# Performance work log

Measured on AMD Instinct MI355X. Metric: run time of the kernel, lower is better.

Reference implementation:

```python
import jax, jax.numpy as jnp
import numpy as np

EPS = 1e-8
MASK_MIN = 0.0


def setup_inputs() -> dict:
    key = jax.random.key(0)
    k1, k2, k3, k4 = jax.random.split(key, 4)
    B, H, CELLS, W = 8, 8, 8192, 256
    memory = jax.random.normal(k1, (B, CELLS, W), dtype=jnp.float32)
    keys = jax.random.normal(k2, (B, H, W), dtype=jnp.float32)
    betas = jax.random.uniform(k3, (B, H), dtype=jnp.float32)
    mask = jax.random.uniform(k4, (B, H, W), dtype=jnp.float32)
    return {"memory": memory, "keys": keys, "betas": betas, "mask": mask}


def reference(memory, keys, betas, mask):
    # memory: [B, C, W]; keys: [B, H, W]; betas: [B, H]; mask: [B, H, W]
    mask = mask * (1.0 - MASK_MIN) + MASK_MIN
    m2 = mask * mask                                   # [B, H, W]
    keys_m = keys * mask                               # masked keys
    # (memory*mask) . (keys*mask) summed over W == memory . (keys*mask^2)
    dots = jnp.einsum('bcw,bhw->bhc', memory, keys * m2)        # [B, H, C]
    keys_norm = jnp.linalg.norm(keys_m, axis=-1)                # [B, H]
    mem_norm = jnp.sqrt(jnp.einsum('bcw,bhw->bhc', memory * memory, m2))  # [B, H, C]
    norm = keys_norm[..., None] * mem_norm                      # [B, H, C]
    scores = dots / (norm + EPS) * betas[..., None]
    return jax.nn.softmax(scores, axis=-1)                      # [B, H, C]
```

## Files before the change

kernel.cpp:

```cpp
#include <hip/hip_runtime.h>
#include <cstdint>
#include <cmath>

#define EPS_F 1e-8f

constexpr int B = 8, H = 8, CELLS = 8192, W = 256;
constexpr int W4 = 64;
constexpr int TC = 32;
constexpr int NBLK = CELLS / TC;

template <int CTRL>
__device__ __forceinline__ float ror_add(float v) {
    int x = __builtin_amdgcn_update_dpp(0, __builtin_bit_cast(int, v),
                                        CTRL, 0xf, 0xf, false);
    return v + __builtin_bit_cast(float, x);
}
__device__ __forceinline__ float row_sum16(float v) {
    v = ror_add<0x121>(v);
    v = ror_add<0x122>(v);
    v = ror_add<0x124>(v);
    v = ror_add<0x128>(v);
    return v;
}

#define GLOAD_LDS16(g, l)                                                    \
    __builtin_amdgcn_global_load_lds(                                        \
        (__attribute__((address_space(1))) void*)(void*)(g),                 \
        (__attribute__((address_space(3))) void*)(l), 16, 0, 0)

__global__ __launch_bounds__(256, 3) void ca_scores(
    const float4* __restrict__ mem4,
    const float4* __restrict__ keys4,
    const float4* __restrict__ mask4,
    const float* __restrict__ betas,
    float* __restrict__ out,
    float2* __restrict__ part)
{
    __shared__ float4 s_tile[TC * W4];
    __shared__ float  s_sc[H][TC + 1];
    __shared__ float  s_fin[H], s_sum2[H];

    const int b = blockIdx.y, blk = blockIdx.x, t = threadIdx.x;
    const int c0 = blk * TC;
    const int lane = t & 63, wv = t >> 6;
    const int hp  = (lane >> 4) & 3;
    const int wsl = lane & 15;

    const float4* __restrict__ kA = keys4 + ((size_t)(b * 8 + hp)) * W4;
    const float4* __restrict__ mA = mask4 + ((size_t)(b * 8 + hp)) * W4;
    const float4* __restrict__ kB = keys4 + ((size_t)(b * 8 + hp + 4)) * W4;
    const float4* __restrict__ mB = mask4 + ((size_t)(b * 8 + hp + 4)) * W4;
    float4 ka[4], ma[4], kb[4], mb[4];
#pragma unroll
    for (int j = 0; j < 4; ++j) {
        ka[j] = kA[j * 16 + wsl];  ma[j] = mA[j * 16 + wsl];
        kb[j] = kB[j * 16 + wsl];  mb[j] = mB[j * 16 + wsl];
    }
    const float beA = betas[b * 8 + hp];
    const float beB = betas[b * 8 + hp + 4];

    const float4* __restrict__ gbase = mem4 + ((size_t)b * CELLS + c0) * W4;
#pragma unroll
    for (int i = 0; i < 8; ++i)
        GLOAD_LDS16(gbase + t + i * 256, &s_tile[t + i * 256]);

    float4 tb[16];
    float pA = 0.f, pB = 0.f;
#pragma unroll
    for (int j = 0; j < 4; ++j) {
        float4 m = ma[j];
        float4 q = make_float4(m.x * m.x, m.y * m.y, m.z * m.z, m.w * m.w);
        float4 k = ka[j];
        tb[j * 4 + 0] = make_float4(k.x * q.x, k.y * q.y, k.z * q.z, k.w * q.w);
        tb[j * 4 + 1] = q;
        float km;
        km = k.x * m.x; pA = fmaf(km, km, pA);
        km = k.y * m.y; pA = fmaf(km, km, pA);
        km = k.z * m.z; pA = fmaf(km, km, pA);
        km = k.w * m.w; pA = fmaf(km, km, pA);
        m = mb[j];
        q = make_float4(m.x * m.x, m.y * m.y, m.z * m.z, m.w * m.w);
        k = kb[j];
        tb[j * 4 + 2] = make_float4(k.x * q.x, k.y * q.y, k.z * q.z, k.w * q.w);
        tb[j * 4 + 3] = q;
        km = k.x * m.x; pB = fmaf(km, km, pB);
        km = k.y * m.y; pB = fmaf(km, km, pB);
        km = k.z * m.z; pB = fmaf(km, km, pB);
        km = k.w * m.w; pB = fmaf(km, km, pB);
    }
    const float knA = sqrtf(row_sum16(pA));
    const float knB = sqrtf(row_sum16(pB));

    __syncthreads();

#pragma unroll
    for (int c = 0; c < 8; ++c) {
        const int cell = wv * 8 + c;
        const float4* __restrict__ pr = s_tile + cell * W4 + wsl;
        float4 a0 = pr[0], a1 = pr[16], a2 = pr[32], a3 = pr[48];

        float4 dA = make_float4(0.f, 0.f, 0.f, 0.f);
        float4 nA = make_float4(0.f, 0.f, 0.f, 0.f);
        float4 dB = make_float4(0.f, 0.f, 0.f, 0.f);
        float4 nB = make_float4(0.f, 0.f, 0.f, 0.f);

#define ACC(a, j)                                                           \
        {                                                                   \
            float4 sq = make_float4(a.x * a.x, a.y * a.y, a.z * a.z, a.w * a.w); \
            float4 kqA = tb[(j) * 4 + 0], qA = tb[(j) * 4 + 1];             \
            float4 kqB = tb[(j) * 4 + 2], qB = tb[(j) * 4 + 3];             \
            dA.x = fmaf(a.x, kqA.x, dA.x); dA.y = fmaf(a.y, kqA.y, dA.y);   \
            dA.z = fmaf(a.z, kqA.z, dA.z); dA.w = fmaf(a.w, kqA.w, dA.w);   \
            nA.x = fmaf(sq.x, qA.x, nA.x); nA.y = fmaf(sq.y, qA.y, nA.y);   \
            nA.z = fmaf(sq.z, qA.z, nA.z); nA.w = fmaf(sq.w, qA.w, nA.w);   \
            dB.x = fmaf(a.x, kqB.x, dB.x); dB.y = fmaf(a.y, kqB.y, dB.y);   \
            dB.z = fmaf(a.z, kqB.z, dB.z); dB.w = fmaf(a.w, kqB.w, dB.w);   \
            nB.x = fmaf(sq.x, qB.x, nB.x); nB.y = fmaf(sq.y, qB.y, nB.y);   \
            nB.z = fmaf(sq.z, qB.z, nB.z); nB.w = fmaf(sq.w, qB.w, nB.w);   \
        }
        ACC(a0, 0) ACC(a1, 1) ACC(a2, 2) ACC(a3, 3)
#undef ACC

        float d0 = (dA.x + dA.y) + (dA.z + dA.w);
        float n0 = (nA.x + nA.y) + (nA.z + nA.w);
        float d1 = (dB.x + dB.y) + (dB.z + dB.w);
        float n1 = (nB.x + nB.y) + (nB.z + nB.w);
        d0 = row_sum16(d0); n0 = row_sum16(n0);
        d1 = row_sum16(d1); n1 = row_sum16(n1);

        float s0 = d0 * beA / (knA * sqrtf(n0) + EPS_F);
        float s1 = d1 * beB / (knB * sqrtf(n1) + EPS_F);
        if (wsl == c) {
            s_sc[hp][cell]     = s0;
            s_sc[hp + 4][cell] = s1;
        }
    }
    __syncthreads();

    const int oh = t >> 5, oc = t & 31;
    float sc = s_sc[oh][oc];
    out[((size_t)(b * H + oh)) * CELLS + c0 + oc] = sc;

    float mx = sc;
#pragma unroll
    for (int s = 1; s <= 16; s <<= 1) mx = fmaxf(mx, __shfl_xor(mx, s, 64));
    float e = expf(sc - mx);
#pragma unroll
    for (int s = 1; s <= 16; s <<= 1) e += __shfl_xor(e, s, 64);
    if (oc == 0) { s_fin[oh] = mx; s_sum2[oh] = e; }
    __syncthreads();
    if (t < H)
        part[((size_t)(b * H + t)) * NBLK + blk] = make_float2(s_fin[t], s_sum2[t]);
}

__global__ __launch_bounds__(256) void ca_norm(
    float* __restrict__ out, const float2* __restrict__ part)
{
    const int row = blockIdx.x >> 3;
    const int seg = blockIdx.x & 7;
    const int t = threadIdx.x, lane = t & 63;

    const float2* __restrict__ pp = part + (size_t)row * NBLK;
    float2 a0 = pp[lane], a1 = pp[lane + 64], a2 = pp[lane + 128], a3 = pp[lane + 192];
    float gm = fmaxf(fmaxf(a0.x, a1.x), fmaxf(a2.x, a3.x));
#pragma unroll
    for (int s = 32; s; s >>= 1) gm = fmaxf(gm, __shfl_xor(gm, s, 64));
    float gs = a0.y * expf(a0.x - gm) + a1.y * expf(a1.x - gm)
             + a2.y * expf(a2.x - gm) + a3.y * expf(a3.x - gm);
#pragma unroll
    for (int s = 32; s; s >>= 1) gs += __shfl_xor(gs, s, 64);
    float inv = 1.0f / gs;

    float4* p = (float4*)(out + (size_t)row * CELLS) + seg * 256;
    float4 vv = p[t];
    vv.x = expf(vv.x - gm) * inv;
    vv.y = expf(vv.y - gm) * inv;
    vv.z = expf(vv.z - gm) * inv;
    vv.w = expf(vv.w - gm) * inv;
    p[t] = vv;
}

extern "C" void kernel_launch(void* const* d_in, const int* in_sizes, int n_in,
                              void* d_out, int out_size, void* d_ws, size_t ws_size,
                              hipStream_t stream) {
    (void)in_sizes; (void)n_in; (void)out_size; (void)ws_size;
    const float* memory = (const float*)d_in[0];
    const float* keys   = (const float*)d_in[1];
    const float* betas  = (const float*)d_in[2];
    const float* mask   = (const float*)d_in[3];
    float* out = (float*)d_out;
    float2* part = (float2*)d_ws;

    dim3 gA(NBLK, B);
    ca_scores<<<gA, 256, 0, stream>>>((const float4*)memory,
                                      (const float4*)keys, (const float4*)mask,
                                      betas, out, part);
    ca_norm<<<8 * B * H, 256, 0, stream>>>(out, part);
}
```

Measured before the change: 31.56 us.

## Double-buffer memory tiles across persistent loop of 16-cell sub-tiles per block

```diff
diff --git a/kernel.cpp b/kernel.cpp
--- a/kernel.cpp
+++ b/kernel.cpp
@@ -6,8 +6,10 @@
 
 constexpr int B = 8, H = 8, CELLS = 8192, W = 256;
 constexpr int W4 = 64;
-constexpr int TC = 32;
+constexpr int TC = 16;
+constexpr int NT = 4;
 constexpr int NBLK = CELLS / TC;
+constexpr int GX = CELLS / (TC * NT);
 
 template <int CTRL>
 __device__ __forceinline__ float ror_add(float v) {
@@ -36,41 +38,25 @@
     float* __restrict__ out,
     float2* __restrict__ part)
 {
-    __shared__ float4 s_tile[TC * W4];
+    __shared__ float4 s_buf[2][TC * W4];
     __shared__ float  s_sc[H][TC + 1];
-    __shared__ float  s_fin[H], s_sum2[H];
-
-    const int b = blockIdx.y, blk = blockIdx.x, t = threadIdx.x;
-    const int c0 = blk * TC;
+
+    const int b = blockIdx.y, grp = blockIdx.x, t = threadIdx.x;
     const int lane = t & 63, wv = t >> 6;
     const int hp  = (lane >> 4) & 3;
     const int wsl = lane & 15;
-
-    const float4* __restrict__ kA = keys4 + ((size_t)(b * 8 + hp)) * W4;
-    const float4* __restrict__ mA = mask4 + ((size_t)(b * 8 + hp)) * W4;
-    const float4* __restrict__ kB = keys4 + ((size_t)(b * 8 + hp + 4)) * W4;
-    const float4* __restrict__ mB = mask4 + ((size_t)(b * 8 + hp + 4)) * W4;
-    float4 ka[4], ma[4], kb[4], mb[4];
-#pragma unroll
-    for (int j = 0; j < 4; ++j) {
-        ka[j] = kA[j * 16 + wsl];  ma[j] = mA[j * 16 + wsl];
-        kb[j] = kB[j * 16 + wsl];  mb[j] = mB[j * 16 + wsl];
-    }
-    const float beA = betas[b * 8 + hp];
-    const float beB = betas[b * 8 + hp + 4];
-
-    const float4* __restrict__ gbase = mem4 + ((size_t)b * CELLS + c0) * W4;
-#pragma unroll
-    for (int i = 0; i < 8; ++i)
-        GLOAD_LDS16(gbase + t + i * 256, &s_tile[t + i * 256]);
-
+    const int c0  = grp * (TC * NT);
+
+    const float4* __restrict__ kA = keys4 + (size_t)(b * 8 + hp) * W4;
+    const float4* __restrict__ mA = mask4 + (size_t)(b * 8 + hp) * W4;
+    const float4* __restrict__ kB = keys4 + (size_t)(b * 8 + hp + 4) * W4;
+    const float4* __restrict__ mB = mask4 + (size_t)(b * 8 + hp + 4) * W4;
     float4 tb[16];
     float pA = 0.f, pB = 0.f;
 #pragma unroll
     for (int j = 0; j < 4; ++j) {
-        float4 m = ma[j];
+        float4 k = kA[j * 16 + wsl], m = mA[j * 16 + wsl];
         float4 q = make_float4(m.x * m.x, m.y * m.y, m.z * m.z, m.w * m.w);
-        float4 k = ka[j];
         tb[j * 4 + 0] = make_float4(k.x * q.x, k.y * q.y, k.z * q.z, k.w * q.w);
         tb[j * 4 + 1] = q;
         float km;
@@ -78,9 +64,8 @@
         km = k.y * m.y; pA = fmaf(km, km, pA);
         km = k.z * m.z; pA = fmaf(km, km, pA);
         km = k.w * m.w; pA = fmaf(km, km, pA);
-        m = mb[j];
+        k = kB[j * 16 + wsl]; m = mB[j * 16 + wsl];
         q = make_float4(m.x * m.x, m.y * m.y, m.z * m.z, m.w * m.w);
-        k = kb[j];
         tb[j * 4 + 2] = make_float4(k.x * q.x, k.y * q.y, k.z * q.z, k.w * q.w);
         tb[j * 4 + 3] = q;
         km = k.x * m.x; pB = fmaf(km, km, pB);
@@ -88,69 +73,93 @@
         km = k.z * m.z; pB = fmaf(km, km, pB);
         km = k.w * m.w; pB = fmaf(km, km, pB);
     }
+    const float beA = betas[b * 8 + hp];
+    const float beB = betas[b * 8 + hp + 4];
+
+    {
+        const float4* __restrict__ g0 = mem4 + ((size_t)b * CELLS + c0) * W4;
+#pragma unroll
+        for (int i = 0; i < 4; ++i)
+            GLOAD_LDS16(g0 + t + i * 256, &s_buf[0][t + i * 256]);
+    }
     const float knA = sqrtf(row_sum16(pA));
     const float knB = sqrtf(row_sum16(pB));
 
-    __syncthreads();
-
-#pragma unroll
-    for (int c = 0; c < 8; ++c) {
-        const int cell = wv * 8 + c;
-        const float4* __restrict__ pr = s_tile + cell * W4 + wsl;
-        float4 a0 = pr[0], a1 = pr[16], a2 = pr[32], a3 = pr[48];
-
-        float4 dA = make_float4(0.f, 0.f, 0.f, 0.f);
-        float4 nA = make_float4(0.f, 0.f, 0.f, 0.f);
-        float4 dB = make_float4(0.f, 0.f, 0.f, 0.f);
-        float4 nB = make_float4(0.f, 0.f, 0.f, 0.f);
+#pragma unroll
+    for (int nt = 0; nt < NT; ++nt) {
+        __syncthreads();
+        const int cur = nt & 1;
+
+        if (nt + 1 < NT) {
+            const float4* __restrict__ gn =
+                mem4 + ((size_t)b * CELLS + c0 + (nt + 1) * TC) * W4;
+#pragma unroll
+            for (int i = 0; i < 4; ++i)
+                GLOAD_LDS16(gn + t + i * 256, &s_buf[cur ^ 1][t + i * 256]);
+        }
+
+#pragma unroll
+        for (int c = 0; c < 4; ++c) {
+            const int cell = wv * 4 + c;
+            const float4* __restrict__ pr = &s_buf[cur][cell * W4 + wsl];
+            float4 a0 = pr[0], a1 = pr[16], a2 = pr[32], a3 = pr[48];
+
+            float4 dA = make_float4(0.f, 0.f, 0.f, 0.f);
+            float4 nA = make_float4(0.f, 0.f, 0.f, 0.f);
+            float4 dB = make_float4(0.f, 0.f, 0.f, 0.f);
+            float4 nB = make_float4(0.f, 0.f, 0.f, 0.f);
 
 #define ACC(a, j)                                                           \
-        {                                                                   \
-            float4 sq = make_float4(a.x * a.x, a.y * a.y, a.z * a.z, a.w * a.w); \
-            float4 kqA = tb[(j) * 4 + 0], qA = tb[(j) * 4 + 1];             \
-            float4 kqB = tb[(j) * 4 + 2], qB = tb[(j) * 4 + 3];             \
-            dA.x = fmaf(a.x, kqA.x, dA.x); dA.y = fmaf(a.y, kqA.y, dA.y);   \
-            dA.z = fmaf(a.z, kqA.z, dA.z); dA.w = fmaf(a.w, kqA.w, dA.w);   \
-            nA.x = fmaf(sq.x, qA.x, nA.x); nA.y = fmaf(sq.y, qA.y, nA.y);   \
-            nA.z = fmaf(sq.z, qA.z, nA.z); nA.w = fmaf(sq.w, qA.w, nA.w);   \
-            dB.x = fmaf(a.x, kqB.x, dB.x); dB.y = fmaf(a.y, kqB.y, dB.y);   \
-            dB.z = fmaf(a.z, kqB.z, dB.z); dB.w = fmaf(a.w, kqB.w, dB.w);   \
-            nB.x = fmaf(sq.x, qB.x, nB.x); nB.y = fmaf(sq.y, qB.y, nB.y);   \
-            nB.z = fmaf(sq.z, qB.z, nB.z); nB.w = fmaf(sq.w, qB.w, nB.w);   \
+            {                                                               \
+                float4 sq = make_float4(a.x * a.x, a.y * a.y, a.z * a.z, a.w * a.w); \
+                float4 kqA = tb[(j) * 4 + 0], qA = tb[(j) * 4 + 1];         \
+                float4 kqB = tb[(j) * 4 + 2], qB = tb[(j) * 4 + 3];         \
+                dA.x = fmaf(a.x, kqA.x, dA.x); dA.y = fmaf(a.y, kqA.y, dA.y); \
+                dA.z = fmaf(a.z, kqA.z, dA.z); dA.w = fmaf(a.w, kqA.w, dA.w); \
+                nA.x = fmaf(sq.x, qA.x, nA.x); nA.y = fmaf(sq.y, qA.y, nA.y); \
+                nA.z = fmaf(sq.z, qA.z, nA.z); nA.w = fmaf(sq.w, qA.w, nA.w); \
+                dB.x = fmaf(a.x, kqB.x, dB.x); dB.y = fmaf(a.y, kqB.y, dB.y); \
+                dB.z = fmaf(a.z, kqB.z, dB.z); dB.w = fmaf(a.w, kqB.w, dB.w); \
+                nB.x = fmaf(sq.x, qB.x, nB.x); nB.y = fmaf(sq.y, qB.y, nB.y); \
+                nB.z = fmaf(sq.z, qB.z, nB.z); nB.w = fmaf(sq.w, qB.w, nB.w); \
+            }
+            ACC(a0, 0) ACC(a1, 1) ACC(a2, 2) ACC(a3, 3)
+#undef ACC
+
+            float d0 = (dA.x + dA.y) + (dA.z + dA.w);
+            float n0 = (nA.x + nA.y) + (nA.z + nA.w);
+            float d1 = (dB.x + dB.y) + (dB.z + dB.w);
+            float n1 = (nB.x + nB.y) + (nB.z + nB.w);
+            d0 = row_sum16(d0); n0 = row_sum16(n0);
+            d1 = row_sum16(d1); n1 = row_sum16(n1);
+
+            float s0 = d0 * beA / (knA * sqrtf(n0) + EPS_F);
+            float s1 = d1 * beB / (knB * sqrtf(n1) + EPS_F);
+            if (wsl == c) {
+                s_sc[hp][cell]     = s0;
+                s_sc[hp + 4][cell] = s1;
+            }
         }
-        ACC(a0, 0) ACC(a1, 1) ACC(a2, 2) ACC(a3, 3)
-#undef ACC
-
-        float d0 = (dA.x + dA.y) + (dA.z + dA.w);
-        float n0 = (nA.x + nA.y) + (nA.z + nA.w);
-        float d1 = (dB.x + dB.y) + (dB.z + dB.w);
-        float n1 = (nB.x + nB.y) + (nB.z + nB.w);
-        d0 = row_sum16(d0); n0 = row_sum16(n0);
-        d1 = row_sum16(d1); n1 = row_sum16(n1);
-
-        float s0 = d0 * beA / (knA * sqrtf(n0) + EPS_F);
-        float s1 = d1 * beB / (knB * sqrtf(n1) + EPS_F);
-        if (wsl == c) {
-            s_sc[hp][cell]     = s0;
-            s_sc[hp + 4][cell] = s1;
+
+        asm volatile("s_waitcnt lgkmcnt(0)" ::: "memory");
+        __builtin_amdgcn_s_barrier();
+        __builtin_amdgcn_sched_barrier(0);
+        if (t < 128) {
+            const int oh = t >> 4, oc = t & 15;
+            float sc = s_sc[oh][oc];
+            out[((size_t)(b * H + oh)) * CELLS + c0 + nt * TC + oc] = sc;
+            float mx = sc;
+#pragma unroll
+            for (int s = 1; s <= 8; s <<= 1) mx = fmaxf(mx, __shfl_xor(mx, s, 64));
+            float e = expf(sc - mx);
+#pragma unroll
+            for (int s = 1; s <= 8; s <<= 1) e += __shfl_xor(e, s, 64);
+            if (oc == 0)
+                part[((size_t)(b * H + oh)) * NBLK + grp * NT + nt] =
+                    make_float2(mx, e);
         }
+        __builtin_amdgcn_sched_barrier(0);
     }
-    __syncthreads();
-
-    const int oh = t >> 5, oc = t & 31;
-    float sc = s_sc[oh][oc];
-    out[((size_t)(b * H + oh)) * CELLS + c0 + oc] = sc;
-
-    float mx = sc;
-#pragma unroll
-    for (int s = 1; s <= 16; s <<= 1) mx = fmaxf(mx, __shfl_xor(mx, s, 64));
-    float e = expf(sc - mx);
-#pragma unroll
-    for (int s = 1; s <= 16; s <<= 1) e += __shfl_xor(e, s, 64);
-    if (oc == 0) { s_fin[oh] = mx; s_sum2[oh] = e; }
-    __syncthreads();
-    if (t < H)
-        part[((size_t)(b * H + t)) * NBLK + blk] = make_float2(s_fin[t], s_sum2[t]);
 }
 
 __global__ __launch_bounds__(256) void ca_norm(
@@ -161,12 +170,17 @@
     const int t = threadIdx.x, lane = t & 63;
 
     const float2* __restrict__ pp = part + (size_t)row * NBLK;
-    float2 a0 = pp[lane], a1 = pp[lane + 64], a2 = pp[lane + 128], a3 = pp[lane + 192];
-    float gm = fmaxf(fmaxf(a0.x, a1.x), fmaxf(a2.x, a3.x));
+    float2 a[8];
+#pragma unroll
+    for (int i = 0; i < 8; ++i) a[i] = pp[lane + i * 64];
+    float gm = -INFINITY;
+#pragma unroll
+    for (int i = 0; i < 8; ++i) gm = fmaxf(gm, a[i].x);
 #pragma unroll
     for (int s = 32; s; s >>= 1) gm = fmaxf(gm, __shfl_xor(gm, s, 64));
-    float gs = a0.y * expf(a0.x - gm) + a1.y * expf(a1.x - gm)
-             + a2.y * expf(a2.x - gm) + a3.y * expf(a3.x - gm);
+    float gs = 0.f;
+#pragma unroll
+    for (int i = 0; i < 8; ++i) gs += a[i].y * expf(a[i].x - gm);
 #pragma unroll
     for (int s = 32; s; s >>= 1) gs += __shfl_xor(gs, s, 64);
     float inv = 1.0f / gs;
@@ -191,7 +205,7 @@
     float* out = (float*)d_out;
     float2* part = (float2*)d_ws;
 
-    dim3 gA(NBLK, B);
+    dim3 gA(GX, B);
     ca_scores<<<gA, 256, 0, stream>>>((const float4*)memory,
                                       (const float4*)keys, (const float4*)mask,
                                       betas, out, part);
```

Result: slower. 32.95 us (+4.4%).

## Replace LDS staging with per-wave register prefetch pipeline and larger cell tiles

Applied to the files above, without the earlier changes.

```diff
diff --git a/kernel.cpp b/kernel.cpp
--- a/kernel.cpp
+++ b/kernel.cpp
@@ -6,8 +6,9 @@
 
 constexpr int B = 8, H = 8, CELLS = 8192, W = 256;
 constexpr int W4 = 64;
-constexpr int TC = 32;
-constexpr int NBLK = CELLS / TC;
+constexpr int CPW = 16;
+constexpr int CPB = 64;
+constexpr int NBLK = CELLS / CPB;
 
 template <int CTRL>
 __device__ __forceinline__ float ror_add(float v) {
@@ -23,11 +24,6 @@
     return v;
 }
 
-#define GLOAD_LDS16(g, l)                                                    \
-    __builtin_amdgcn_global_load_lds(                                        \
-        (__attribute__((address_space(1))) void*)(void*)(g),                 \
-        (__attribute__((address_space(3))) void*)(l), 16, 0, 0)
-
 __global__ __launch_bounds__(256, 3) void ca_scores(
     const float4* __restrict__ mem4,
     const float4* __restrict__ keys4,
@@ -36,20 +32,19 @@
     float* __restrict__ out,
     float2* __restrict__ part)
 {
-    __shared__ float4 s_tile[TC * W4];
-    __shared__ float  s_sc[H][TC + 1];
-    __shared__ float  s_fin[H], s_sum2[H];
+    __shared__ float s_sc[H][CPB + 1];
 
     const int b = blockIdx.y, blk = blockIdx.x, t = threadIdx.x;
-    const int c0 = blk * TC;
     const int lane = t & 63, wv = t >> 6;
     const int hp  = (lane >> 4) & 3;
     const int wsl = lane & 15;
+    const int c0  = blk * CPB;
+    const int cw0 = c0 + wv * CPW;
 
-    const float4* __restrict__ kA = keys4 + ((size_t)(b * 8 + hp)) * W4;
-    const float4* __restrict__ mA = mask4 + ((size_t)(b * 8 + hp)) * W4;
-    const float4* __restrict__ kB = keys4 + ((size_t)(b * 8 + hp + 4)) * W4;
-    const float4* __restrict__ mB = mask4 + ((size_t)(b * 8 + hp + 4)) * W4;
+    const float4* __restrict__ kA = keys4 + (size_t)(b * 8 + hp) * W4;
+    const float4* __restrict__ mA = mask4 + (size_t)(b * 8 + hp) * W4;
+    const float4* __restrict__ kB = keys4 + (size_t)(b * 8 + hp + 4) * W4;
+    const float4* __restrict__ mB = mask4 + (size_t)(b * 8 + hp + 4) * W4;
     float4 ka[4], ma[4], kb[4], mb[4];
 #pragma unroll
     for (int j = 0; j < 4; ++j) {
@@ -59,18 +54,22 @@
     const float beA = betas[b * 8 + hp];
     const float beB = betas[b * 8 + hp + 4];
 
-    const float4* __restrict__ gbase = mem4 + ((size_t)b * CELLS + c0) * W4;
-#pragma unroll
-    for (int i = 0; i < 8; ++i)
-        GLOAD_LDS16(gbase + t + i * 256, &s_tile[t + i * 256]);
+    const float4* __restrict__ gro =
+        mem4 + ((size_t)b * CELLS + cw0) * W4 + wsl;
+    float4 pf[3][4];
+#define LOADC(slot, i)                                                       \
+    { const float4* __restrict__ p = gro + (i) * W4;                         \
+      pf[slot][0] = p[0];  pf[slot][1] = p[16];                              \
+      pf[slot][2] = p[32]; pf[slot][3] = p[48]; }
+    LOADC(0, 0)
+    LOADC(1, 1)
 
     float4 tb[16];
     float pA = 0.f, pB = 0.f;
 #pragma unroll
     for (int j = 0; j < 4; ++j) {
-        float4 m = ma[j];
+        float4 m = ma[j], k = ka[j];
         float4 q = make_float4(m.x * m.x, m.y * m.y, m.z * m.z, m.w * m.w);
-        float4 k = ka[j];
         tb[j * 4 + 0] = make_float4(k.x * q.x, k.y * q.y, k.z * q.z, k.w * q.w);
         tb[j * 4 + 1] = q;
         float km;
@@ -78,9 +77,8 @@
         km = k.y * m.y; pA = fmaf(km, km, pA);
         km = k.z * m.z; pA = fmaf(km, km, pA);
         km = k.w * m.w; pA = fmaf(km, km, pA);
-        m = mb[j];
+        m = mb[j]; k = kb[j];
         q = make_float4(m.x * m.x, m.y * m.y, m.z * m.z, m.w * m.w);
-        k = kb[j];
         tb[j * 4 + 2] = make_float4(k.x * q.x, k.y * q.y, k.z * q.z, k.w * q.w);
         tb[j * 4 + 3] = q;
         km = k.x * m.x; pB = fmaf(km, km, pB);
@@ -91,19 +89,14 @@
     const float knA = sqrtf(row_sum16(pA));
     const float knB = sqrtf(row_sum16(pB));
 
-    __syncthreads();
-
 #pragma unroll
-    for (int c = 0; c < 8; ++c) {
-        const int cell = wv * 8 + c;
-        const float4* __restrict__ pr = s_tile + cell * W4 + wsl;
-        float4 a0 = pr[0], a1 = pr[16], a2 = pr[32], a3 = pr[48];
+    for (int i = 0; i < CPW; ++i) {
+        if (i + 2 < CPW) LOADC((i + 2) % 3, i + 2)
 
         float4 dA = make_float4(0.f, 0.f, 0.f, 0.f);
         float4 nA = make_float4(0.f, 0.f, 0.f, 0.f);
         float4 dB = make_float4(0.f, 0.f, 0.f, 0.f);
         float4 nB = make_float4(0.f, 0.f, 0.f, 0.f);
-
 #define ACC(a, j)                                                           \
         {                                                                   \
             float4 sq = make_float4(a.x * a.x, a.y * a.y, a.z * a.z, a.w * a.w); \
@@ -118,7 +111,10 @@
             nB.x = fmaf(sq.x, qB.x, nB.x); nB.y = fmaf(sq.y, qB.y, nB.y);   \
             nB.z = fmaf(sq.z, qB.z, nB.z); nB.w = fmaf(sq.w, qB.w, nB.w);   \
         }
-        ACC(a0, 0) ACC(a1, 1) ACC(a2, 2) ACC(a3, 3)
+        ACC(pf[i % 3][0], 0)
+        ACC(pf[i % 3][1], 1)
+        ACC(pf[i % 3][2], 2)
+        ACC(pf[i % 3][3], 3)
 #undef ACC
 
         float d0 = (dA.x + dA.y) + (dA.z + dA.w);
@@ -130,27 +126,29 @@
 
         float s0 = d0 * beA / (knA * sqrtf(n0) + EPS_F);
         float s1 = d1 * beB / (knB * sqrtf(n1) + EPS_F);
-        if (wsl == c) {
-            s_sc[hp][cell]     = s0;
-            s_sc[hp + 4][cell] = s1;
+        if (wsl == i) {
+            s_sc[hp][wv * CPW + i]     = s0;
+            s_sc[hp + 4][wv * CPW + i] = s1;
         }
     }
+#undef LOADC
     __syncthreads();
 
     const int oh = t >> 5, oc = t & 31;
-    float sc = s_sc[oh][oc];
-    out[((size_t)(b * H + oh)) * CELLS + c0 + oc] = sc;
+    float sc0 = s_sc[oh][oc];
+    float sc1 = s_sc[oh][oc + 32];
+    const size_t orow = ((size_t)(b * H + oh)) * CELLS + c0;
+    out[orow + oc]      = sc0;
+    out[orow + oc + 32] = sc1;
 
-    float mx = sc;
+    float mx = fmaxf(sc0, sc1);
 #pragma unroll
     for (int s = 1; s <= 16; s <<= 1) mx = fmaxf(mx, __shfl_xor(mx, s, 64));
-    float e = expf(sc - mx);
+    float e = expf(sc0 - mx) + expf(sc1 - mx);
 #pragma unroll
     for (int s = 1; s <= 16; s <<= 1) e += __shfl_xor(e, s, 64);
-    if (oc == 0) { s_fin[oh] = mx; s_sum2[oh] = e; }
-    __syncthreads();
-    if (t < H)
-        part[((size_t)(b * H + t)) * NBLK + blk] = make_float2(s_fin[t], s_sum2[t]);
+    if (oc == 0)
+        part[((size_t)(b * H + oh)) * NBLK + blk] = make_float2(mx, e);
 }
 
 __global__ __launch_bounds__(256) void ca_norm(
@@ -161,12 +159,11 @@
     const int t = threadIdx.x, lane = t & 63;
 
     const float2* __restrict__ pp = part + (size_t)row * NBLK;
-    float2 a0 = pp[lane], a1 = pp[lane + 64], a2 = pp[lane + 128], a3 = pp[lane + 192];
-    float gm = fmaxf(fmaxf(a0.x, a1.x), fmaxf(a2.x, a3.x));
+    float2 a0 = pp[lane], a1 = pp[lane + 64];
+    float gm = fmaxf(a0.x, a1.x);
 #pragma unroll
     for (int s = 32; s; s >>= 1) gm = fmaxf(gm, __shfl_xor(gm, s, 64));
-    float gs = a0.y * expf(a0.x - gm) + a1.y * expf(a1.x - gm)
-             + a2.y * expf(a2.x - gm) + a3.y * expf(a3.x - gm);
+    float gs = a0.y * expf(a0.x - gm) + a1.y * expf(a1.x - gm);
 #pragma unroll
     for (int s = 32; s; s >>= 1) gs += __shfl_xor(gs, s, 64);
     float inv = 1.0f / gs;
```

New measurement: 29.21 us. -7.4%, faster.
